# Kernel tuning notes

Measured on AMD Instinct MI355X. Metric: run time of the kernel, lower is better.

## Reference

```python
import jax, jax.numpy as jnp
import numpy as np

R = 8192        # proposals per image
D = 4096        # box-head feature dim (input_shape.channels)
C = 80          # num_classes (COCO)
K_PRE = 512     # per-class pre-NMS top-k candidates
IMG_W, IMG_H = 1000.0, 800.0
SCORE_THRESH = 1e-5
NMS_THRESH = 0.5
TOPK = 100      # test_topk_per_image


def setup_inputs() -> dict:
    key = jax.random.key(0)
    ks = jax.random.split(key, 6)
    x = jax.random.normal(ks[0], (R, D), jnp.float32)
    # Xavier-uniform init for the two linear heads
    lim = np.sqrt(6.0 / (D + C)).astype(np.float32)
    Wc = jax.random.uniform(ks[1], (D, C), jnp.float32, -lim, lim)
    bc = jnp.zeros((C,), jnp.float32)
    Wd = jax.random.uniform(ks[2], (D, C), jnp.float32, -lim, lim)
    bd = jnp.zeros((C,), jnp.float32)
    # class-agnostic proposal boxes in xyxy, roughly inside the image
    xy = jax.random.uniform(ks[3], (R, 2), jnp.float32) * jnp.array([IMG_W * 0.8, IMG_H * 0.8], jnp.float32)
    wh = jax.random.uniform(ks[4], (R, 2), jnp.float32) * jnp.array([IMG_W * 0.3, IMG_H * 0.3], jnp.float32) + 4.0
    boxes = jnp.concatenate([xy, xy + wh], axis=1)
    return {"x": x, "Wc": Wc, "bc": bc, "Wd": Wd, "bd": bd, "boxes": boxes}


def _pairwise_iou(b):  # b: [K,4] xyxy -> [K,K]
    area = (b[:, 2] - b[:, 0]) * (b[:, 3] - b[:, 1])
    lt = jnp.maximum(b[:, None, :2], b[None, :, :2])
    rb = jnp.minimum(b[:, None, 2:], b[None, :, 2:])
    wh = jnp.clip(rb - lt, 0.0)
    inter = wh[..., 0] * wh[..., 1]
    return inter / (area[:, None] + area[None, :] - inter + 1e-9)


def _nms_one_class(scores_c, boxes):  # scores_c: [R], boxes: [R,4] -> keep mask [R]
    vals, idx = jax.lax.top_k(scores_c, K_PRE)          # pre-NMS top-k, score-sorted desc
    iou = _pairwise_iou(boxes[idx])                      # [K_PRE, K_PRE]
    valid = vals > SCORE_THRESH                          # score thresholding

    def body(kept, i):
        # suppressed if any already-kept higher-scoring box overlaps too much
        sup = jnp.any(kept & (iou[i] > NMS_THRESH))
        k = valid[i] & (~sup)
        return kept.at[i].set(k), k

    _, keeps = jax.lax.scan(body, jnp.zeros((K_PRE,), bool), jnp.arange(K_PRE))
    return jnp.zeros((scores_c.shape[0],), bool).at[idx].set(keeps)


def _clip_boxes(boxes):
    x1 = jnp.clip(boxes[:, 0:1], 0.0, IMG_W)
    y1 = jnp.clip(boxes[:, 1:2], 0.0, IMG_H)
    x2 = jnp.clip(boxes[:, 2:3], 0.0, IMG_W)
    y2 = jnp.clip(boxes[:, 3:4], 0.0, IMG_H)
    return jnp.concatenate([x1, y1, x2, y2], axis=1)


def reference(x, Wc, bc, Wd, bd, boxes):
    # WSDDN-style object-mining head: softmax over classes x softmax over proposals
    cls_logits = x @ Wc + bc                    # [R, C]
    det_logits = x @ Wd + bd                    # [R, C]
    pred = jax.nn.softmax(cls_logits, axis=1) * jax.nn.softmax(det_logits, axis=0)

    # inference path: clip boxes, threshold, per-class (batched) NMS, keep topk
    bclip = _clip_boxes(boxes)
    keep = jax.vmap(_nms_one_class, in_axes=(1, None), out_axes=1)(pred, bclip)  # [R, C]
    kept_scores = jnp.where(keep, pred, 0.0)
    # topk_per_image across all (proposal, class) detections
    kth = jax.lax.top_k(kept_scores.reshape(-1), TOPK)[0][-1]
    return jnp.where(kept_scores >= kth, kept_scores, 0.0)   # [R, C]
```

## Files before the change

### kernel.cpp

```cpp
#include <hip/hip_runtime.h>
#include <hip/hip_bf16.h>
#include <math.h>

#define R_N 8192
#define D_K 4096
#define C_N 80
#define NC2 160
#define KSPLIT 8
#define KSLICE (D_K / KSPLIT)
#define KPRE 512
#define TOPK 100
#define LIST_CAP (80 * 512)

typedef _Float16 f16;
typedef f16 f16x2 __attribute__((ext_vector_type(2)));
typedef f16 f16x8 __attribute__((ext_vector_type(8)));
typedef float f32x4 __attribute__((ext_vector_type(4)));
typedef unsigned long long u64;

__device__ __forceinline__ void async_copy16(const void* g, void* l) {
    __builtin_amdgcn_global_load_lds(
        (const __attribute__((address_space(1))) void*)g,
        (__attribute__((address_space(3))) void*)l, 16, 0, 0);
}

__global__ __launch_bounds__(256) void init_kernel(const float* __restrict__ Wc,
                                                   const float* __restrict__ Wd,
                                                   float* __restrict__ out,
                                                   unsigned* __restrict__ cnt,
                                                   f16* __restrict__ BhT,
                                                   f16* __restrict__ BlT) {
    const int b = blockIdx.x, tid = threadIdx.x;
    if (b < 640) {
        ((float4*)out)[b * 256 + tid] = make_float4(0.f, 0.f, 0.f, 0.f);
        if (b == 0 && tid == 0) *cnt = 0u;
        return;
    }
    __shared__ float Ws[32 * 161];
    const int kb = b - 640;
    const int k0 = kb * 32;
    for (int i = tid; i < 1280; i += 256) {
        int row = i / 40, q = i % 40;
        const float* src = (q < 20) ? (Wc + (size_t)(k0 + row) * C_N + q * 4)
                                    : (Wd + (size_t)(k0 + row) * C_N + (q - 20) * 4);
        float4 t4 = *(const float4*)src;
        int cc = (q < 20) ? q * 4 : 80 + (q - 20) * 4;
        Ws[row * 161 + cc + 0] = t4.x; Ws[row * 161 + cc + 1] = t4.y;
        Ws[row * 161 + cc + 2] = t4.z; Ws[row * 161 + cc + 3] = t4.w;
    }
    __syncthreads();
    const int g = tid >> 4, l = tid & 15;
#pragma unroll
    for (int p = 0; p < 10; ++p) {
        int n = p * 16 + g;
        float v0 = Ws[(2 * l) * 161 + n];
        float v1 = Ws[(2 * l + 1) * 161 + n];
        f16 h0 = (f16)v0, h1 = (f16)v1;
        f16 l0 = (f16)(v0 - (float)h0), l1 = (f16)(v1 - (float)h1);
        *(f16x2*)&BhT[(size_t)n * D_K + k0 + 2 * l] = (f16x2){h0, h1};
        *(f16x2*)&BlT[(size_t)n * D_K + k0 + 2 * l] = (f16x2){l0, l1};
    }
}

__global__ __launch_bounds__(256) void gemm_part(const float* __restrict__ x,
                                                 const f16* __restrict__ BhT,
                                                 const f16* __restrict__ BlT,
                                                 float* __restrict__ part) {
    __shared__ __align__(16) float As[128 * 32];
    __shared__ __align__(16) f16 Bhs[160 * 32];
    __shared__ __align__(16) f16 Bls[160 * 32];

    const int b    = blockIdx.x;
    const int rb   = b & 63;
    const int ks   = b >> 6;
    const int row0 = rb * 128;
    const int kbase = ks * KSLICE;
    const int tid  = threadIdx.x;
    const int wv   = tid >> 6, lane = tid & 63;
    const int wm   = wv & 1, wn = wv >> 1;
    const int m    = lane & 15, quad = lane >> 4;

    f32x4 acc[4][5];
#pragma unroll
    for (int t = 0; t < 4; ++t)
#pragma unroll
        for (int n = 0; n < 5; ++n) acc[t][n] = (f32x4)(0.0f);

    for (int ch = 0; ch < KSLICE / 32; ++ch) {
        const int k0 = kbase + ch * 32;
#pragma unroll
        for (int i = 0; i < 4; ++i) {
            int t = tid + 256 * i;
            int r = t >> 3, cs = t & 7;
            int cg = cs ^ (r & 7);
            async_copy16(x + (size_t)(row0 + r) * D_K + k0 + cg * 4,
                         (char*)As + (size_t)t * 16);
        }
#pragma unroll
        for (int i = 0; i < 3; ++i) {
            int t = tid + 256 * i;
            if (t < 640) {
                int nn = t >> 2, cc = t & 3;
                size_t go = (size_t)nn * D_K + k0 + cc * 8;
                async_copy16(BhT + go, (char*)Bhs + (size_t)t * 16);
                async_copy16(BlT + go, (char*)Bls + (size_t)t * 16);
            }
        }
        __syncthreads();
        f16x8 ah[4], al[4];
#pragma unroll
        for (int t = 0; t < 4; ++t) {
            int r = wm * 64 + t * 16 + m;
            int r7 = r & 7;
            float4 c0 = *(const float4*)&As[r * 32 + (((2 * quad) ^ r7) << 2)];
            float4 c1 = *(const float4*)&As[r * 32 + (((2 * quad + 1) ^ r7) << 2)];
            float tv[8] = {c0.x, c0.y, c0.z, c0.w, c1.x, c1.y, c1.z, c1.w};
#pragma unroll
            for (int j = 0; j < 8; ++j) {
                f16 h = (f16)tv[j];
                ah[t][j] = h;
                al[t][j] = (f16)(tv[j] - (float)h);
            }
        }
#pragma unroll
        for (int n = 0; n < 5; ++n) {
            int nn = (wn * 5 + n) * 16 + m;
            f16x8 bh = *(const f16x8*)&Bhs[nn * 32 + quad * 8];
            f16x8 bl = *(const f16x8*)&Bls[nn * 32 + quad * 8];
#pragma unroll
            for (int t = 0; t < 4; ++t) {
                acc[t][n] = __builtin_amdgcn_mfma_f32_16x16x32_f16(al[t], bh, acc[t][n], 0, 0, 0);
                acc[t][n] = __builtin_amdgcn_mfma_f32_16x16x32_f16(ah[t], bl, acc[t][n], 0, 0, 0);
                acc[t][n] = __builtin_amdgcn_mfma_f32_16x16x32_f16(ah[t], bh, acc[t][n], 0, 0, 0);
            }
        }
        __syncthreads();
    }
#pragma unroll
    for (int t = 0; t < 4; ++t) {
        int grow0 = row0 + wm * 64 + t * 16 + quad * 4;
#pragma unroll
        for (int n = 0; n < 5; ++n) {
            int gcol = (wn * 5 + n) * 16 + m;
#pragma unroll
            for (int r4 = 0; r4 < 4; ++r4)
                part[((size_t)ks * R_N + grow0 + r4) * NC2 + gcol] = acc[t][n][r4];
        }
    }
}

__global__ __launch_bounds__(256) void reduce_bias(const float* __restrict__ part,
                                                   const float* __restrict__ bc,
                                                   const float* __restrict__ bd,
                                                   float* __restrict__ cls,
                                                   float* __restrict__ detT) {
    const size_t STRIDE = (size_t)R_N * NC2;
    size_t idx = (size_t)blockIdx.x * 256 + threadIdx.x;
    int row = (int)(idx / NC2), col = (int)(idx % NC2);
    float p0 = part[idx + 0 * STRIDE], p1 = part[idx + 1 * STRIDE];
    float p2 = part[idx + 2 * STRIDE], p3 = part[idx + 3 * STRIDE];
    float p4 = part[idx + 4 * STRIDE], p5 = part[idx + 5 * STRIDE];
    float p6 = part[idx + 6 * STRIDE], p7 = part[idx + 7 * STRIDE];
    float s = ((p0 + p1) + (p2 + p3)) + ((p4 + p5) + (p6 + p7));
    if (col < C_N) {
        cls[(size_t)row * C_N + col] = s + bc[col];
    } else {
        detT[(size_t)(col - C_N) * R_N + row] = s + bd[col - C_N];
    }
}

__global__ __launch_bounds__(256) void row_softmax(const float* __restrict__ cls,
                                                   float* __restrict__ Pt) {
    int tid = threadIdx.x;
    int wave = tid >> 6, lane = tid & 63;
    int row = blockIdx.x * 4 + wave;
    float v0 = cls[(size_t)row * C_N + lane];
    float v1 = (lane < 16) ? cls[(size_t)row * C_N + 64 + lane] : -INFINITY;
    float m = fmaxf(v0, v1);
#pragma unroll
    for (int off = 32; off > 0; off >>= 1) m = fmaxf(m, __shfl_xor(m, off, 64));
    float e0 = expf(v0 - m);
    float e1 = (lane < 16) ? expf(v1 - m) : 0.0f;
    float s = e0 + e1;
#pragma unroll
    for (int off = 32; off > 0; off >>= 1) s += __shfl_xor(s, off, 64);
    Pt[(size_t)lane * R_N + row] = e0 / s;
    if (lane < 16) Pt[(size_t)(64 + lane) * R_N + row] = e1 / s;
}

__global__ __launch_bounds__(256) void col_stats(const float* __restrict__ detT,
                                                 float* __restrict__ cm,
                                                 float* __restrict__ csum) {
    __shared__ float red[256];
    int c = blockIdx.x, tid = threadIdx.x;
    const float* dc = detT + (size_t)c * R_N;
    float m = -INFINITY;
    for (int r = tid; r < R_N; r += 256) m = fmaxf(m, dc[r]);
    red[tid] = m; __syncthreads();
    for (int s2 = 128; s2 > 0; s2 >>= 1) {
        if (tid < s2) red[tid] = fmaxf(red[tid], red[tid + s2]);
        __syncthreads();
    }
    m = red[0]; __syncthreads();
    float sum = 0.0f;
    for (int r = tid; r < R_N; r += 256) sum += expf(dc[r] - m);
    red[tid] = sum; __syncthreads();
    for (int s2 = 128; s2 > 0; s2 >>= 1) {
        if (tid < s2) red[tid] += red[tid + s2];
        __syncthreads();
    }
    if (tid == 0) { cm[c] = m; csum[c] = red[0]; }
}

__global__ __launch_bounds__(256) void chunk_sort(const float* __restrict__ Pt,
                                                  const float* __restrict__ detT,
                                                  const float* __restrict__ cm,
                                                  const float* __restrict__ csum,
                                                  unsigned long long* __restrict__ cand) {
    __shared__ u64 sk[1024];
    const int c = blockIdx.x >> 3, ch = blockIdx.x & 7;
    const int tid = threadIdx.x;
    const float m = cm[c], s = csum[c];
    const float* pc = Pt + (size_t)c * R_N + ch * 1024;
    const float* dc = detT + (size_t)c * R_N + ch * 1024;

    for (int i = tid; i < 1024; i += 256) {
        float val = pc[i] * (expf(dc[i] - m) / s);
        unsigned u = __float_as_uint(val);
        int r = ch * 1024 + i;
        sk[i] = ((u64)u << 32) | (unsigned)(8191 - r);
    }
    __syncthreads();
    for (int size = 2; size <= 1024; size <<= 1) {
        for (int stride = size >> 1; stride > 0; stride >>= 1) {
            for (int t = tid; t < 512; t += 256) {
                int i = 2 * t - (t & (stride - 1));
                int j = i + stride;
                u64 a = sk[i], b = sk[j];
                bool desc = ((i & size) == 0);
                if ((a < b) == desc) { sk[i] = b; sk[j] = a; }
            }
            __syncthreads();
        }
    }
    u64* dst = cand + (size_t)blockIdx.x * 512;
    for (int i = tid; i < 512; i += 256) dst[i] = sk[i];
}

__global__ __launch_bounds__(256) void merge_nms(const u64* __restrict__ cand,
                                                 const float* __restrict__ boxes,
                                                 float* __restrict__ g_ls,
                                                 unsigned* __restrict__ g_lp,
                                                 unsigned* __restrict__ g_cnt,
                                                 float* __restrict__ k100) {
    __shared__ u64 A[1024];
    __shared__ float sx1[512], sy1[512], sx2[512], sy2[512], sar[512], svals[512];
    __shared__ int sridx[512];
    __shared__ u64 msk[512 * 8];
    __shared__ unsigned char keepf[512];
    __shared__ int s_nv;

    const int c = blockIdx.x, tid = threadIdx.x;
    const u64* base = cand + (size_t)c * 8 * 512;

    for (int i = tid; i < 512; i += 256) A[i] = base[i];
    for (int l2 = 1; l2 < 8; ++l2) {
        __syncthreads();
        for (int i = tid; i < 512; i += 256) A[512 + i] = base[l2 * 512 + (511 - i)];
        __syncthreads();
        for (int stride = 512; stride > 0; stride >>= 1) {
            for (int t = tid; t < 512; t += 256) {
                int i = 2 * t - (t & (stride - 1));
                int j = i + stride;
                u64 a = A[i], b = A[j];
                if (a < b) { A[i] = b; A[j] = a; }
            }
            __syncthreads();
        }
    }
    __syncthreads();
    for (int i = tid; i < 512; i += 256) {
        u64 k = A[i];
        float v = __uint_as_float((unsigned)(k >> 32));
        int r = 8191 - (int)(k & 0xFFFFFFFFull);
        svals[i] = v; sridx[i] = r;
        float b0 = boxes[r * 4 + 0], b1 = boxes[r * 4 + 1];
        float b2 = boxes[r * 4 + 2], b3 = boxes[r * 4 + 3];
        float x1 = fminf(fmaxf(b0, 0.0f), 1000.0f);
        float y1 = fminf(fmaxf(b1, 0.0f), 800.0f);
        float x2 = fminf(fmaxf(b2, 0.0f), 1000.0f);
        float y2 = fminf(fmaxf(b3, 0.0f), 800.0f);
        sx1[i] = x1; sy1[i] = y1; sx2[i] = x2; sy2[i] = y2;
        sar[i] = (x2 - x1) * (y2 - y1);
        float vn = (i < 511) ? __uint_as_float((unsigned)(A[i + 1] >> 32)) : -1.0f;
        if (v > 1e-5f && !(vn > 1e-5f)) s_nv = i + 1;
        if (i == 0 && !(v > 1e-5f)) s_nv = 0;
    }
    __syncthreads();
    const int nv = s_nv;
    for (int task = tid; task < 512 * 8; task += 256) {
        int i = task >> 3, w = task & 7;
        u64 bits = 0ull;
        if (i < nv && w <= (i >> 6)) {
            float xi1 = sx1[i], yi1 = sy1[i], xi2 = sx2[i], yi2 = sy2[i], ai = sar[i];
#pragma unroll 8
            for (int j2 = 0; j2 < 64; ++j2) {
                int j = (w << 6) + j2;
                float xx1 = fmaxf(xi1, sx1[j]);
                float yy1 = fmaxf(yi1, sy1[j]);
                float xx2 = fminf(xi2, sx2[j]);
                float yy2 = fminf(yi2, sy2[j]);
                float ww = fmaxf(xx2 - xx1, 0.0f);
                float hh = fmaxf(yy2 - yy1, 0.0f);
                float inter = ww * hh;
                float iou = inter / (ai + sar[j] - inter + 1e-9f);
                if (iou > 0.5f) bits |= (1ull << j2);
            }
        }
        msk[i * 8 + w] = bits;
    }
    __syncthreads();
    if (tid < 64) {
        const int lane = tid;
        const bool rd = (lane < 8);
        u64 keptw = 0ull;
        u64 pf[8];
#pragma unroll
        for (int d = 0; d < 8; ++d) pf[d] = rd ? msk[(d & 511) * 8 + lane] : 0ull;
        for (int i = 0; i < nv; ++i) {
            u64 mm = pf[i & 7];
            int ip = (i + 8) & 511;
            pf[i & 7] = rd ? msk[ip * 8 + lane] : 0ull;
            int sup = __any((keptw & mm) != 0ull);
            int keep = !sup;
            if (keep && lane == (i >> 6)) keptw |= (1ull << (i & 63));
            if (lane == 0) keepf[i] = (unsigned char)keep;
        }
        for (int i = lane; i < 100; i += 64) k100[c * 100 + i] = 0.0f;
        unsigned base2 = 0;
        for (int ch2 = 0; ch2 < 8 && (int)base2 < 100; ++ch2) {
            int i = ch2 * 64 + lane;
            bool kk = (i < nv) && (keepf[i] != 0);
            u64 mb = __ballot(kk);
            unsigned pre = (unsigned)__popcll(mb & ((1ull << lane) - 1ull));
            if (kk && base2 + pre < 100)
                k100[c * 100 + base2 + pre] = svals[i];
            base2 += (unsigned)__popcll(mb);
        }
    }
    __syncthreads();
    for (int i = tid; i < nv; i += 256) {
        if (keepf[i]) {
            unsigned pos = atomicAdd(g_cnt, 1u);
            g_ls[pos] = svals[i];
            g_lp[pos] = (unsigned)(sridx[i] * C_N + c);
        }
    }
}

__global__ __launch_bounds__(256) void kth_kernel(const float* __restrict__ k100,
                                                  float* __restrict__ g_kth) {
    __shared__ unsigned red[4];
    __shared__ unsigned s_total;
    const int tid = threadIdx.x;
    const int wv = tid >> 6, lane = tid & 63;
    unsigned v[32];
#pragma unroll
    for (int j = 0; j < 32; ++j) {
        int idx = j * 256 + tid;
        v[j] = (idx < C_N * 100) ? __float_as_uint(k100[idx]) : 0u;
    }
    unsigned lo = 0u, hi = 0x7FFFFFFFu;
    while (lo < hi) {
        unsigned mid = lo + (hi - lo + 1) / 2;
        unsigned cnt = 0;
#pragma unroll
        for (int j = 0; j < 32; ++j) cnt += (v[j] >= mid) ? 1u : 0u;
#pragma unroll
        for (int off = 32; off > 0; off >>= 1) cnt += __shfl_down(cnt, off, 64);
        if (lane == 0) red[wv] = cnt;
        __syncthreads();
        if (tid == 0) s_total = red[0] + red[1] + red[2] + red[3];
        __syncthreads();
        unsigned total = s_total;
        if (total >= (unsigned)TOPK) lo = mid; else hi = mid - 1;
    }
    if (tid == 0) *g_kth = __uint_as_float(lo);
}

__global__ __launch_bounds__(256) void scatter_kernel(const float* __restrict__ g_ls,
                                                      const unsigned* __restrict__ g_lp,
                                                      const unsigned* __restrict__ g_cnt,
                                                      const float* __restrict__ g_kth,
                                                      float* __restrict__ out) {
    unsigned idx = blockIdx.x * 256 + threadIdx.x;
    unsigned n = *g_cnt;
    float kth = *g_kth;
    if (idx < n) {
        float s = g_ls[idx];
        if (s >= kth) out[g_lp[idx]] = s;
    }
}

extern "C" void kernel_launch(void* const* d_in, const int* in_sizes, int n_in,
                              void* d_out, int out_size, void* d_ws, size_t ws_size,
                              hipStream_t stream) {
    const float* x     = (const float*)d_in[0];
    const float* Wc    = (const float*)d_in[1];
    const float* bc    = (const float*)d_in[2];
    const float* Wd    = (const float*)d_in[3];
    const float* bd    = (const float*)d_in[4];
    const float* boxes = (const float*)d_in[5];
    float* out = (float*)d_out;

    char* w = (char*)d_ws;
    float* part = (float*)w;  w += (size_t)KSPLIT * R_N * NC2 * sizeof(float);
    float* cls  = (float*)w;  w += (size_t)R_N * C_N * sizeof(float);
    float* detT = (float*)w;  w += (size_t)C_N * R_N * sizeof(float);
    float* Pt   = (float*)w;  w += (size_t)C_N * R_N * sizeof(float);
    float* g_ls = (float*)w;  w += (size_t)LIST_CAP * sizeof(float);
    unsigned* g_lp = (unsigned*)w; w += (size_t)LIST_CAP * sizeof(unsigned);
    unsigned* g_cnt = (unsigned*)w; w += 256;
    float* g_kth = (float*)w; w += 256;
    f16* BhT = (f16*)w; w += (size_t)NC2 * D_K * sizeof(f16);
    f16* BlT = (f16*)w; w += (size_t)NC2 * D_K * sizeof(f16);
    float* k100 = (float*)w; w += (size_t)C_N * 100 * sizeof(float);
    float* cm   = (float*)w; w += 1024;
    float* csum = (float*)w; w += 1024;

    u64* cand = (u64*)part;

    init_kernel<<<768, 256, 0, stream>>>(Wc, Wd, out, g_cnt, BhT, BlT);
    gemm_part<<<64 * KSPLIT, 256, 0, stream>>>(x, BhT, BlT, part);
    reduce_bias<<<(R_N * NC2) / 256, 256, 0, stream>>>(part, bc, bd, cls, detT);
    row_softmax<<<R_N / 4, 256, 0, stream>>>(cls, Pt);
    col_stats<<<C_N, 256, 0, stream>>>(detT, cm, csum);
    chunk_sort<<<C_N * 8, 256, 0, stream>>>(Pt, detT, cm, csum, cand);
    merge_nms<<<C_N, 256, 0, stream>>>(cand, boxes, g_ls, g_lp, g_cnt, k100);
    kth_kernel<<<1, 256, 0, stream>>>(k100, g_kth);
    scatter_kernel<<<(LIST_CAP + 255) / 256, 256, 0, stream>>>(g_ls, g_lp, g_cnt, g_kth, out);
}
```

Measured before the change: 404.9 us.

## Split per-class merge+NMS kernel into staged kernels with wider parallelism

Replaces the single 80-block merge_nms kernel with four kernels. A 320-block first merge level runs, then a 4-way merge with box extraction, then a 640-block IoU mask kernel, then a one-wave-per-class sequential NMS scan. The aim is to spread the merge and the IoU mask computation across more CUs, since with one block per class the GPU was underused. In exchange it adds three extra launches and sends intermediates (candidates, boxes, masks) through global memory instead of LDS.

```diff
diff --git a/kernel.cpp b/kernel.cpp
--- a/kernel.cpp
+++ b/kernel.cpp
@@ -216,7 +216,7 @@
                                                   const float* __restrict__ detT,
                                                   const float* __restrict__ cm,
                                                   const float* __restrict__ csum,
-                                                  unsigned long long* __restrict__ cand) {
+                                                  u64* __restrict__ cand) {
     __shared__ u64 sk[1024];
     const int c = blockIdx.x >> 3, ch = blockIdx.x & 7;
     const int tid = threadIdx.x;
@@ -247,26 +247,45 @@
     for (int i = tid; i < 512; i += 256) dst[i] = sk[i];
 }
 
-__global__ __launch_bounds__(256) void merge_nms(const u64* __restrict__ cand,
-                                                 const float* __restrict__ boxes,
-                                                 float* __restrict__ g_ls,
-                                                 unsigned* __restrict__ g_lp,
-                                                 unsigned* __restrict__ g_cnt,
-                                                 float* __restrict__ k100) {
+__global__ __launch_bounds__(256) void merge4(const u64* __restrict__ cand,
+                                              u64* __restrict__ cand2) {
     __shared__ u64 A[1024];
-    __shared__ float sx1[512], sy1[512], sx2[512], sy2[512], sar[512], svals[512];
-    __shared__ int sridx[512];
-    __shared__ u64 msk[512 * 8];
-    __shared__ unsigned char keepf[512];
-    __shared__ int s_nv;
-
+    const int c = blockIdx.x >> 2, q = blockIdx.x & 3;
+    const int tid = threadIdx.x;
+    const u64* b0 = cand + ((size_t)c * 8 + 2 * q) * 512;
+    const u64* b1 = cand + ((size_t)c * 8 + 2 * q + 1) * 512;
+    for (int i = tid; i < 512; i += 256) {
+        A[i] = b0[i];
+        A[512 + i] = b1[511 - i];
+    }
+    __syncthreads();
+    for (int stride = 512; stride > 0; stride >>= 1) {
+        for (int t = tid; t < 512; t += 256) {
+            int i = 2 * t - (t & (stride - 1));
+            int j = i + stride;
+            u64 a = A[i], b = A[j];
+            if (a < b) { A[i] = b; A[j] = a; }
+        }
+        __syncthreads();
+    }
+    u64* dst = cand2 + ((size_t)c * 4 + q) * 512;
+    for (int i = tid; i < 512; i += 256) dst[i] = A[i];
+}
+
+__global__ __launch_bounds__(256) void merge_extract4(const u64* __restrict__ cand2,
+                                                      const float* __restrict__ boxes,
+                                                      float* __restrict__ svals,
+                                                      int* __restrict__ sridx,
+                                                      float* __restrict__ cbox,
+                                                      int* __restrict__ nvalid) {
+    __shared__ u64 A[1024];
     const int c = blockIdx.x, tid = threadIdx.x;
-    const u64* base = cand + (size_t)c * 8 * 512;
+    const u64* base = cand2 + (size_t)c * 4 * 512;
 
     for (int i = tid; i < 512; i += 256) A[i] = base[i];
-    for (int l2 = 1; l2 < 8; ++l2) {
-        __syncthreads();
-        for (int i = tid; i < 512; i += 256) A[512 + i] = base[l2 * 512 + (511 - i)];
+    for (int l = 1; l < 4; ++l) {
+        __syncthreads();
+        for (int i = tid; i < 512; i += 256) A[512 + i] = base[l * 512 + (511 - i)];
         __syncthreads();
         for (int stride = 512; stride > 0; stride >>= 1) {
             for (int t = tid; t < 512; t += 256) {
@@ -283,23 +302,37 @@
         u64 k = A[i];
         float v = __uint_as_float((unsigned)(k >> 32));
         int r = 8191 - (int)(k & 0xFFFFFFFFull);
-        svals[i] = v; sridx[i] = r;
+        svals[c * 512 + i] = v;
+        sridx[c * 512 + i] = r;
         float b0 = boxes[r * 4 + 0], b1 = boxes[r * 4 + 1];
         float b2 = boxes[r * 4 + 2], b3 = boxes[r * 4 + 3];
-        float x1 = fminf(fmaxf(b0, 0.0f), 1000.0f);
-        float y1 = fminf(fmaxf(b1, 0.0f), 800.0f);
-        float x2 = fminf(fmaxf(b2, 0.0f), 1000.0f);
-        float y2 = fminf(fmaxf(b3, 0.0f), 800.0f);
-        sx1[i] = x1; sy1[i] = y1; sx2[i] = x2; sy2[i] = y2;
-        sar[i] = (x2 - x1) * (y2 - y1);
+        float4 cb;
+        cb.x = fminf(fmaxf(b0, 0.0f), 1000.0f);
+        cb.y = fminf(fmaxf(b1, 0.0f), 800.0f);
+        cb.z = fminf(fmaxf(b2, 0.0f), 1000.0f);
+        cb.w = fminf(fmaxf(b3, 0.0f), 800.0f);
+        *(float4*)&cbox[((size_t)c * 512 + i) * 4] = cb;
         float vn = (i < 511) ? __uint_as_float((unsigned)(A[i + 1] >> 32)) : -1.0f;
-        if (v > 1e-5f && !(vn > 1e-5f)) s_nv = i + 1;
-        if (i == 0 && !(v > 1e-5f)) s_nv = 0;
-    }
-    __syncthreads();
-    const int nv = s_nv;
-    for (int task = tid; task < 512 * 8; task += 256) {
-        int i = task >> 3, w = task & 7;
+        if (v > 1e-5f && !(vn > 1e-5f)) nvalid[c] = i + 1;
+        if (i == 0 && !(v > 1e-5f)) nvalid[c] = 0;
+    }
+}
+
+__global__ __launch_bounds__(256) void iou_mask(const float* __restrict__ cbox,
+                                                const int* __restrict__ nvalid,
+                                                u64* __restrict__ gmask) {
+    __shared__ float sx1[512], sy1[512], sx2[512], sy2[512], sar[512];
+    const int c = blockIdx.x >> 3, w = blockIdx.x & 7;
+    const int tid = threadIdx.x;
+    const int nv = nvalid[c];
+
+    for (int i = tid; i < 512; i += 256) {
+        float4 b = *(const float4*)&cbox[((size_t)c * 512 + i) * 4];
+        sx1[i] = b.x; sy1[i] = b.y; sx2[i] = b.z; sy2[i] = b.w;
+        sar[i] = (b.z - b.x) * (b.w - b.y);
+    }
+    __syncthreads();
+    for (int i = tid; i < 512; i += 256) {
         u64 bits = 0ull;
         if (i < nv && w <= (i >> 6)) {
             float xi1 = sx1[i], yi1 = sy1[i], xi2 = sx2[i], yi2 = sy2[i], ai = sar[i];
@@ -317,44 +350,59 @@
                 if (iou > 0.5f) bits |= (1ull << j2);
             }
         }
-        msk[i * 8 + w] = bits;
-    }
-    __syncthreads();
-    if (tid < 64) {
-        const int lane = tid;
-        const bool rd = (lane < 8);
-        u64 keptw = 0ull;
-        u64 pf[8];
-#pragma unroll
-        for (int d = 0; d < 8; ++d) pf[d] = rd ? msk[(d & 511) * 8 + lane] : 0ull;
-        for (int i = 0; i < nv; ++i) {
-            u64 mm = pf[i & 7];
-            int ip = (i + 8) & 511;
-            pf[i & 7] = rd ? msk[ip * 8 + lane] : 0ull;
-            int sup = __any((keptw & mm) != 0ull);
-            int keep = !sup;
-            if (keep && lane == (i >> 6)) keptw |= (1ull << (i & 63));
-            if (lane == 0) keepf[i] = (unsigned char)keep;
-        }
-        for (int i = lane; i < 100; i += 64) k100[c * 100 + i] = 0.0f;
-        unsigned base2 = 0;
-        for (int ch2 = 0; ch2 < 8 && (int)base2 < 100; ++ch2) {
-            int i = ch2 * 64 + lane;
-            bool kk = (i < nv) && (keepf[i] != 0);
-            u64 mb = __ballot(kk);
-            unsigned pre = (unsigned)__popcll(mb & ((1ull << lane) - 1ull));
-            if (kk && base2 + pre < 100)
-                k100[c * 100 + base2 + pre] = svals[i];
-            base2 += (unsigned)__popcll(mb);
-        }
-    }
-    __syncthreads();
-    for (int i = tid; i < nv; i += 256) {
+        gmask[((size_t)c * 512 + i) * 8 + w] = bits;
+    }
+}
+
+__global__ __launch_bounds__(64) void nms_scan(const u64* __restrict__ gmask,
+                                               const float* __restrict__ svals,
+                                               const int* __restrict__ sridx,
+                                               const int* __restrict__ nvalid,
+                                               float* __restrict__ g_ls,
+                                               unsigned* __restrict__ g_lp,
+                                               unsigned* __restrict__ g_cnt,
+                                               float* __restrict__ k100) {
+    __shared__ u64 sm[512 * 8];
+    __shared__ unsigned char keepf[512];
+    const int c = blockIdx.x, lane = threadIdx.x;
+    const int nv = nvalid[c];
+    const u64* gm = gmask + (size_t)c * 512 * 8;
+
+    for (int t = lane; t < 4096; t += 64) sm[t] = gm[t];
+    __syncthreads();
+
+    const bool rd = (lane < 8);
+    u64 keptw = 0ull;
+    u64 pf[8];
+#pragma unroll
+    for (int d = 0; d < 8; ++d) pf[d] = rd ? sm[(d & 511) * 8 + lane] : 0ull;
+    for (int i = 0; i < nv; ++i) {
+        u64 mm = pf[i & 7];
+        int ip = (i + 8) & 511;
+        pf[i & 7] = rd ? sm[ip * 8 + lane] : 0ull;
+        int sup = __any((keptw & mm) != 0ull);
+        int keep = !sup;
+        if (keep && lane == (i >> 6)) keptw |= (1ull << (i & 63));
+        if (lane == 0) keepf[i] = (unsigned char)keep;
+    }
+    __syncthreads();
+    for (int i = lane; i < nv; i += 64) {
         if (keepf[i]) {
             unsigned pos = atomicAdd(g_cnt, 1u);
-            g_ls[pos] = svals[i];
-            g_lp[pos] = (unsigned)(sridx[i] * C_N + c);
-        }
+            g_ls[pos] = svals[c * 512 + i];
+            g_lp[pos] = (unsigned)(sridx[c * 512 + i] * C_N + c);
+        }
+    }
+    for (int i = lane; i < 100; i += 64) k100[c * 100 + i] = 0.0f;
+    unsigned base = 0;
+    for (int ch2 = 0; ch2 < 8 && (int)base < 100; ++ch2) {
+        int i = ch2 * 64 + lane;
+        bool kk = (i < nv) && (keepf[i] != 0);
+        u64 mb = __ballot(kk);
+        unsigned pre = (unsigned)__popcll(mb & ((1ull << lane) - 1ull));
+        if (kk && base + pre < 100)
+            k100[c * 100 + base + pre] = svals[c * 512 + i];
+        base += (unsigned)__popcll(mb);
     }
 }
 
@@ -428,7 +476,14 @@
     float* cm   = (float*)w; w += 1024;
     float* csum = (float*)w; w += 1024;
 
-    u64* cand = (u64*)part;
+    char* a = (char*)part;
+    u64* cand  = (u64*)a; a += (size_t)C_N * 8 * 512 * sizeof(u64);
+    u64* cand2 = (u64*)a; a += (size_t)C_N * 4 * 512 * sizeof(u64);
+    float* svals = (float*)a;  a += (size_t)C_N * KPRE * sizeof(float);
+    int*   sridx = (int*)a;    a += (size_t)C_N * KPRE * sizeof(int);
+    float* cbox  = (float*)a;  a += (size_t)C_N * KPRE * 4 * sizeof(float);
+    int*   nvalid = (int*)a;   a += 4096;
+    u64* gmask = (u64*)a; a += (size_t)C_N * KPRE * 8 * sizeof(u64);
 
     init_kernel<<<768, 256, 0, stream>>>(Wc, Wd, out, g_cnt, BhT, BlT);
     gemm_part<<<64 * KSPLIT, 256, 0, stream>>>(x, BhT, BlT, part);
@@ -436,7 +491,10 @@
     row_softmax<<<R_N / 4, 256, 0, stream>>>(cls, Pt);
     col_stats<<<C_N, 256, 0, stream>>>(detT, cm, csum);
     chunk_sort<<<C_N * 8, 256, 0, stream>>>(Pt, detT, cm, csum, cand);
-    merge_nms<<<C_N, 256, 0, stream>>>(cand, boxes, g_ls, g_lp, g_cnt, k100);
+    merge4<<<C_N * 4, 256, 0, stream>>>(cand, cand2);
+    merge_extract4<<<C_N, 256, 0, stream>>>(cand2, boxes, svals, sridx, cbox, nvalid);
+    iou_mask<<<C_N * 8, 256, 0, stream>>>(cbox, nvalid, gmask);
+    nms_scan<<<C_N, 64, 0, stream>>>(gmask, svals, sridx, nvalid, g_ls, g_lp, g_cnt, k100);
     kth_kernel<<<1, 256, 0, stream>>>(k100, g_kth);
     scatter_kernel<<<(LIST_CAP + 255) / 256, 256, 0, stream>>>(g_ls, g_lp, g_cnt, g_kth, out);
 }
```

Result: faster. 377.6 us (-6.8%).
